# Kernel tuning notes

Hardware: AMD Instinct MI355X
Metric: run time of the kernel (lower is better)

## Reference

```python
import jax, jax.numpy as jnp
import numpy as np

INF = 1.0e9
# 8-connected neighborhood (Warcraft shortest-path convention)
DIRS = [(-1, -1), (-1, 0), (-1, 1), (0, -1), (0, 1), (1, -1), (1, 0), (1, 1)]


def _shifted(d_KGG, di, dj):
    # shifted[i, j] = d[i + di, j + dj], INF out of bounds (di, dj static ints)
    K, G, _ = d_KGG.shape
    p = jnp.pad(d_KGG, ((0, 0), (1, 1), (1, 1)), constant_values=INF)
    return p[:, 1 + di:1 + di + G, 1 + dj:1 + dj + G]


def compute_shortest_path(cost_KGG):
    """Vertex-cost shortest path from (0,0) to (G-1,G-1) on an 8-connected grid.
    Returns a 0/1 mask of cells on the optimal path. Bellman-Ford style DP:
    G*G relaxation sweeps guarantee convergence for positive costs."""
    K, G, _ = cost_KGG.shape
    dist0 = jnp.full((K, G, G), INF, dtype=cost_KGG.dtype).at[:, 0, 0].set(cost_KGG[:, 0, 0])

    def relax(_, dist):
        nbr = dist  # placeholder; fold min over 8 shifted copies
        nbr = _shifted(dist, *DIRS[0])
        for d in DIRS[1:]:
            nbr = jnp.minimum(nbr, _shifted(dist, *d))
        return jnp.minimum(dist, cost_KGG + nbr)

    dist = jax.lax.fori_loop(0, G * G, relax, dist0)

    # Backtrack from (G-1, G-1): predecessor = argmin dist over 8 neighbors.
    di = jnp.array([d[0] for d in DIRS])
    dj = jnp.array([d[1] for d in DIRS])
    ks = jnp.arange(K)

    def step(carry, _):
        mask, pi, pj = carry
        ci = pi[:, None] + di[None, :]   # [K, 8]
        cj = pj[:, None] + dj[None, :]
        valid = (ci >= 0) & (ci < G) & (cj >= 0) & (cj < G)
        cic = jnp.clip(ci, 0, G - 1)
        cjc = jnp.clip(cj, 0, G - 1)
        nd = jnp.where(valid, dist[ks[:, None], cic, cjc], INF)
        best = jnp.argmin(nd, axis=-1)  # [K]
        npi = jnp.take_along_axis(cic, best[:, None], 1)[:, 0]
        npj = jnp.take_along_axis(cjc, best[:, None], 1)[:, 0]
        done = (pi == 0) & (pj == 0)
        pi2 = jnp.where(done, pi, npi)
        pj2 = jnp.where(done, pj, npj)
        mask2 = mask.at[ks, pi2, pj2].set(1.0)
        return (mask2, pi2, pj2), None

    mask0 = jnp.zeros((K, G, G), jnp.float32).at[:, G - 1, G - 1].set(1.0)
    p0 = jnp.full((K,), G - 1, dtype=jnp.int32)
    (mask, _, _), _ = jax.lax.scan(step, (mask0, p0, p0), None, length=G * G)
    return mask


def setup_inputs() -> dict:
    key = jax.random.key(0)
    S, B, G, n_costs = 8, 1024, 12, 5
    w_SBW = jax.random.randint(jax.random.fold_in(key, 1), (S, B, G * G), 0, n_costs)
    costs_t = jnp.array([0.8, 1.2, 5.3, 7.7, 9.2], dtype=jnp.float32)
    return {"w_SBW": w_SBW, "costs_t": costs_t}


def reference(w_SBW, costs_t):
    S, B, W = w_SBW.shape
    G = int(np.sqrt(W))
    w_KGG = w_SBW.reshape(S * B, G, G)
    cost_KGG = costs_t[w_KGG]          # embedding-style gather of per-cell costs
    y_KGG = compute_shortest_path(cost_KGG)
    return y_KGG.reshape(S, B, W).astype(jnp.int32)  # .long() in the original
```

## Files before the change

### kernel.cpp

```cpp
#include <hip/hip_runtime.h>
#include <float.h>

#define GDIM 12
#define NC   144
#define FINF 1.0e9f

__device__ __constant__ int POFF[8] = {-15, -14, -13, -1, 1, 13, 14, 15};

template<int CTRL>
__device__ inline float rot(float x) {
    return __int_as_float(__builtin_amdgcn_update_dpp(
        __float_as_int(x), __float_as_int(x), CTRL, 0xf, 0xf, false));
}

#define ROWU(i, C, D) {                                                    \
    float dm1 = ((i) > 0)        ? D[(i) > 0 ? (i)-1 : 0]        : FINF;   \
    float dp1 = ((i) < GDIM - 1) ? D[(i) < GDIM-1 ? (i)+1 : GDIM-1] : FINF;\
    float V   = fminf(dm1, dp1);                                           \
    float cm3 = fminf(V, D[(i)]);                                          \
    float nbr = fminf(fminf(rot<0x121>(cm3), rot<0x12F>(cm3)), V);         \
    D[(i)] = fminf(D[(i)], C[(i)] + nbr); }

#define SWEEP_DN(C, D) { _Pragma("unroll")                                 \
    for (int i = 0; i < GDIM; ++i) ROWU(i, C, D) }
#define SWEEP_UP(C, D) { _Pragma("unroll")                                 \
    for (int q = 0; q < GDIM; ++q) { const int i = GDIM - 1 - q; ROWU(i, C, D) } }

__global__ __launch_bounds__(64)
void path_kernel(const int* __restrict__ w,
                 const float* __restrict__ costs,
                 int* __restrict__ out) {
    const int l = threadIdx.x;
    const int g = l >> 4;
    const int j = l & 15;
    const int pbase = blockIdx.x * 4;

    __shared__ int4  s_w4[NC];
    __shared__ float dl[4][200];
    __shared__ int4  ml4[NC];
    int* s_w = (int*)s_w4;
    int* ml  = (int*)ml4;

    const float cv0 = costs[0], cv1 = costs[1], cv2 = costs[2],
                cv3 = costs[3], cv4 = costs[4];

    const int4* wv = (const int4*)(w + (size_t)pbase * NC);
    const int4 zero4 = make_int4(0, 0, 0, 0);
    s_w4[l] = wv[l];            ml4[l] = zero4;
    s_w4[64 + l] = wv[64 + l];  ml4[64 + l] = zero4;
    if (l < 16) { s_w4[128 + l] = wv[128 + l]; ml4[128 + l] = zero4; }
    {
        float* dlf = &dl[0][0];
        #pragma unroll
        for (int t = 0; t < 13; ++t) { int idx = t * 64 + l; if (idx < 800) dlf[idx] = FINF; }
    }
    __syncthreads();

    const bool act = (j < GDIM);
    float* A = &dl[g][0];

    float c[GDIM], ct[GDIM], d[GDIM];
    #pragma unroll
    for (int i = 0; i < GDIM; ++i) {
        int wiN = s_w[g * NC + i * GDIM + (act ? j : 0)];
        int idxT = act ? (g * NC + j * GDIM + i) : 0;
        int wiT = s_w[idxT];
        float cN = cv4, cT = cv4;
        cN = (wiN == 0) ? cv0 : cN;  cT = (wiT == 0) ? cv0 : cT;
        cN = (wiN == 1) ? cv1 : cN;  cT = (wiT == 1) ? cv1 : cT;
        cN = (wiN == 2) ? cv2 : cN;  cT = (wiT == 2) ? cv2 : cT;
        cN = (wiN == 3) ? cv3 : cN;  cT = (wiT == 3) ? cv3 : cT;
        c[i]  = act ? cN : FINF;
        ct[i] = act ? cT : FINF;
        d[i] = FINF;
    }
    if (j == 0) d[0] = c[0];

    for (int cyc = 0; cyc < 40; ++cyc) {
        float dp[GDIM];
        #pragma unroll
        for (int i = 0; i < GDIM; ++i) dp[i] = d[i];

        SWEEP_DN(c, d)
        SWEEP_UP(c, d)

        if (act) {
            #pragma unroll
            for (int i = 0; i < GDIM; ++i) A[(i + 1) * 14 + (j + 1)] = d[i];
            #pragma unroll
            for (int i = 0; i < GDIM; ++i) d[i] = A[(j + 1) * 14 + (i + 1)];
        }

        SWEEP_DN(ct, d)
        SWEEP_UP(ct, d)

        if (act) {
            #pragma unroll
            for (int i = 0; i < GDIM; ++i) A[(j + 1) * 14 + (i + 1)] = d[i];
            #pragma unroll
            for (int i = 0; i < GDIM; ++i) d[i] = A[(i + 1) * 14 + (j + 1)];
        }

        bool ch = false;
        #pragma unroll
        for (int i = 0; i < GDIM; ++i) ch = ch | (d[i] < dp[i]);
        if (__ballot(ch) == 0ull) break;
    }
    __syncthreads();

    if (j == 0) {
        int a = 12 * 14 + 12;
        ml[g * NC + NC - 1] = 1;
        int guard = 0;
        while (a != (1 * 14 + 1) && guard < 200) {
            ++guard;
            float best = FLT_MAX; int ba = a;
            #pragma unroll
            for (int dd = 0; dd < 8; ++dd) {
                int na = a + POFF[dd];
                float v = dl[g][na];
                if (v < best) { best = v; ba = na; }
            }
            a = ba;
            int ii = a / 14 - 1, jj = a % 14 - 1;
            ml[g * NC + ii * GDIM + jj] = 1;
        }
    }
    __syncthreads();

    int4* ov = (int4*)(out + (size_t)pbase * NC);
    ov[l] = ml4[l];
    ov[64 + l] = ml4[64 + l];
    if (l < 16) ov[128 + l] = ml4[128 + l];
}

extern "C" void kernel_launch(void* const* d_in, const int* in_sizes, int n_in,
                              void* d_out, int out_size, void* d_ws, size_t ws_size,
                              hipStream_t stream) {
    const int*   w     = (const int*)d_in[0];
    const float* costs = (const float*)d_in[1];
    int*         out   = (int*)d_out;
    const int K = in_sizes[0] / NC;
    path_kernel<<<dim3(K / 4), dim3(64), 0, stream>>>(w, costs, out);
}
```

Baseline: 24.96 us.

## Pack four wavefronts per block and parallelize backtrack across lanes

Blocks now hold 256 threads, four independent wavefronts each solving four grids with private shared-memory slices, so block-wide __syncthreads are dropped. The serial single-lane backtrack is replaced by one where 8 lanes per grid load neighbor distances and a DPP min-reduction plus ballot picks the predecessor. Global loads are issued early into registers, before the cost constants and shared-memory initialization. This targets serial backtrack latency and per-block launch overhead, at the cost of higher shared memory per block and possibly different argmin tie-breaking.

```diff
diff --git a/kernel.cpp b/kernel.cpp
--- a/kernel.cpp
+++ b/kernel.cpp
@@ -4,8 +4,6 @@
 #define GDIM 12
 #define NC   144
 #define FINF 1.0e9f
-
-__device__ __constant__ int POFF[8] = {-15, -14, -13, -1, 1, 13, 14, 15};
 
 template<int CTRL>
 __device__ inline float rot(float x) {
@@ -26,45 +24,49 @@
 #define SWEEP_UP(C, D) { _Pragma("unroll")                                 \
     for (int q = 0; q < GDIM; ++q) { const int i = GDIM - 1 - q; ROWU(i, C, D) } }
 
-__global__ __launch_bounds__(64)
+__global__ __launch_bounds__(256)
 void path_kernel(const int* __restrict__ w,
                  const float* __restrict__ costs,
                  int* __restrict__ out) {
-    const int l = threadIdx.x;
-    const int g = l >> 4;
-    const int j = l & 15;
-    const int pbase = blockIdx.x * 4;
+    const int t  = threadIdx.x;
+    const int wv = t >> 6;
+    const int l  = t & 63;
+    const int g  = l >> 4;
+    const int j  = l & 15;
+    const int pw = blockIdx.x * 16 + wv * 4;
 
-    __shared__ int4  s_w4[NC];
-    __shared__ float dl[4][200];
-    __shared__ int4  ml4[NC];
-    int* s_w = (int*)s_w4;
-    int* ml  = (int*)ml4;
+    __shared__ int4  s_w4[4][NC];
+    __shared__ float dl[4][4][200];
+    __shared__ int   ml[4][4 * NC];
+
+    const int4* wvp = (const int4*)(w + (size_t)pw * NC);
+    int4 wA = wvp[l];
+    int4 wB = wvp[64 + l];
+    int4 wC = (l < 16) ? wvp[128 + l] : make_int4(0, 0, 0, 0);
 
     const float cv0 = costs[0], cv1 = costs[1], cv2 = costs[2],
                 cv3 = costs[3], cv4 = costs[4];
 
-    const int4* wv = (const int4*)(w + (size_t)pbase * NC);
-    const int4 zero4 = make_int4(0, 0, 0, 0);
-    s_w4[l] = wv[l];            ml4[l] = zero4;
-    s_w4[64 + l] = wv[64 + l];  ml4[64 + l] = zero4;
-    if (l < 16) { s_w4[128 + l] = wv[128 + l]; ml4[128 + l] = zero4; }
-    {
-        float* dlf = &dl[0][0];
-        #pragma unroll
-        for (int t = 0; t < 13; ++t) { int idx = t * 64 + l; if (idx < 800) dlf[idx] = FINF; }
-    }
-    __syncthreads();
+    int* mlw = ml[wv];
+    #pragma unroll
+    for (int q = 0; q < 9; ++q) mlw[q * 64 + l] = 0;
+    float* dlw = &dl[wv][0][0];
+    #pragma unroll
+    for (int q = 0; q < 13; ++q) { int idx = q * 64 + l; if (idx < 800) dlw[idx] = FINF; }
+
+    s_w4[wv][l] = wA;
+    s_w4[wv][64 + l] = wB;
+    if (l < 16) s_w4[wv][128 + l] = wC;
 
     const bool act = (j < GDIM);
-    float* A = &dl[g][0];
+    const int* sw = (const int*)s_w4[wv];
+    float* A = &dl[wv][g][0];
 
     float c[GDIM], ct[GDIM], d[GDIM];
     #pragma unroll
     for (int i = 0; i < GDIM; ++i) {
-        int wiN = s_w[g * NC + i * GDIM + (act ? j : 0)];
-        int idxT = act ? (g * NC + j * GDIM + i) : 0;
-        int wiT = s_w[idxT];
+        int wiN = sw[g * NC + i * GDIM + (act ? j : 0)];
+        int wiT = sw[act ? (g * NC + j * GDIM + i) : 0];
         float cN = cv4, cT = cv4;
         cN = (wiN == 0) ? cv0 : cN;  cT = (wiT == 0) ? cv0 : cT;
         cN = (wiN == 1) ? cv1 : cN;  cT = (wiT == 1) ? cv1 : cT;
@@ -72,7 +74,7 @@
         cN = (wiN == 3) ? cv3 : cN;  cT = (wiT == 3) ? cv3 : cT;
         c[i]  = act ? cN : FINF;
         ct[i] = act ? cT : FINF;
-        d[i] = FINF;
+        d[i]  = FINF;
     }
     if (j == 0) d[0] = c[0];
 
@@ -106,32 +108,41 @@
         for (int i = 0; i < GDIM; ++i) ch = ch | (d[i] < dp[i]);
         if (__ballot(ch) == 0ull) break;
     }
-    __syncthreads();
 
-    if (j == 0) {
+    {
+        int* mlg = mlw + g * NC;
+        const int offj = (j < 3) ? (j - 15) : (j == 3) ? -1 : (j == 4) ? 1 : (j + 8);
         int a = 12 * 14 + 12;
-        ml[g * NC + NC - 1] = 1;
-        int guard = 0;
-        while (a != (1 * 14 + 1) && guard < 200) {
-            ++guard;
-            float best = FLT_MAX; int ba = a;
-            #pragma unroll
-            for (int dd = 0; dd < 8; ++dd) {
-                int na = a + POFF[dd];
-                float v = dl[g][na];
-                if (v < best) { best = v; ba = na; }
+        int n = NC - 1;
+        if (j == 0) mlg[n] = 1;
+        const int target = 1 * 14 + 1;
+        for (int s = 0; s < NC; ++s) {
+            if (__ballot(a != target) == 0ull) break;
+            float v = (j < 8) ? A[a + offj] : FINF;
+            float m = v;
+            m = fminf(m, rot<0xB1>(m));
+            m = fminf(m, rot<0x4E>(m));
+            m = fminf(m, rot<0x141>(m));
+            m = fminf(m, rot<0x140>(m));
+            unsigned long long bal = __ballot((j < 8) & (v == m));
+            int mask8 = (int)(bal >> (g * 16)) & 0xFF;
+            int bidx = __ffs(mask8) - 1;
+            if (a != target) {
+                int off = (bidx < 3) ? (bidx - 15) : (bidx == 3) ? -1
+                        : (bidx == 4) ? 1 : (bidx + 8);
+                int adj = (bidx < 3) ? 2 : (bidx > 4) ? -2 : 0;
+                a += off;
+                n += off + adj;
+                if (j == 0) mlg[n] = 1;
             }
-            a = ba;
-            int ii = a / 14 - 1, jj = a % 14 - 1;
-            ml[g * NC + ii * GDIM + jj] = 1;
         }
     }
-    __syncthreads();
 
-    int4* ov = (int4*)(out + (size_t)pbase * NC);
-    ov[l] = ml4[l];
-    ov[64 + l] = ml4[64 + l];
-    if (l < 16) ov[128 + l] = ml4[128 + l];
+    int4* ov = (int4*)(out + (size_t)pw * NC);
+    const int4* ml4w = (const int4*)mlw;
+    ov[l] = ml4w[l];
+    ov[64 + l] = ml4w[64 + l];
+    if (l < 16) ov[128 + l] = ml4w[128 + l];
 }
 
 extern "C" void kernel_launch(void* const* d_in, const int* in_sizes, int n_in,
@@ -141,5 +152,5 @@
     const float* costs = (const float*)d_in[1];
     int*         out   = (int*)d_out;
     const int K = in_sizes[0] / NC;
-    path_kernel<<<dim3(K / 4), dim3(64), 0, stream>>>(w, costs, out);
+    path_kernel<<<dim3(K / 16), dim3(256), 0, stream>>>(w, costs, out);
 }
```

New measurement: 20.92 us. 16.2% less time.
